# Optimization experiments

Measured on AMD Instinct MI355X. Metric: run time of the kernel, lower is better.

## Reference

```python
import jax, jax.numpy as jnp
import numpy as np

N_USERS = 60000
N_ITEMS = 30000
N_NODES = N_USERS + N_ITEMS
D = 64
L = 2


def _norm_adj(edge_index):
    # symmetrize: A_idx = [e, e.flip(0)]
    src = jnp.concatenate([edge_index[0], edge_index[1]])
    dst = jnp.concatenate([edge_index[1], edge_index[0]])
    ones = jnp.ones_like(src, dtype=jnp.float32)
    deg = jax.ops.segment_sum(ones, src, num_segments=N_NODES)
    deg = jnp.clip(deg, 1.0, None)
    val = jax.lax.rsqrt(deg[src]) * jax.lax.rsqrt(deg[dst])
    return src, dst, val


def _spmm(src, dst, val, x):
    # out[i] = sum_{(i,j) in E} val_ij * x[j]
    return jax.ops.segment_sum(val[:, None] * x[dst], src, num_segments=N_NODES)


def setup_inputs() -> dict:
    key = jax.random.key(0)
    ks = jax.random.split(key, 20)
    s = 0.02
    inp = {
        'x_txt': jax.random.normal(ks[0], (N_ITEMS, 768), jnp.float32),
        'x_img': jax.random.normal(ks[1], (N_ITEMS, 512), jnp.float32),
        'x_struct': jax.random.normal(ks[2], (N_ITEMS, 128), jnp.float32),
        'user_emb': jax.random.normal(ks[3], (3, N_USERS, D), jnp.float32) * s,
        'W_txt': jax.random.normal(ks[4], (3, 768, D), jnp.float32) * s,
        'b_txt': jax.random.normal(ks[5], (3, D), jnp.float32) * s,
        'W_img': jax.random.normal(ks[6], (3, 512, D), jnp.float32) * s,
        'b_img': jax.random.normal(ks[7], (3, D), jnp.float32) * s,
        'W_st': jax.random.normal(ks[8], (3, 128, D), jnp.float32) * s,
        'b_st': jax.random.normal(ks[9], (3, D), jnp.float32) * s,
        'Wu1': jax.random.normal(ks[10], (3 * D, 128), jnp.float32) * s,
        'bu1': jax.random.normal(ks[11], (128,), jnp.float32) * s,
        'Wu2': jax.random.normal(ks[12], (128, 3), jnp.float32) * s,
        'bu2': jax.random.normal(ks[13], (3,), jnp.float32) * s,
        'Wi1': jax.random.normal(ks[14], (3 * D, 128), jnp.float32) * s,
        'bi1': jax.random.normal(ks[15], (128,), jnp.float32) * s,
        'Wi2': jax.random.normal(ks[16], (128, 3), jnp.float32) * s,
        'bi2': jax.random.normal(ks[17], (3,), jnp.float32) * s,
        'edge_index': jax.random.randint(ks[18], (2, 500000), 0, N_NODES, jnp.int64),
    }
    return inp


def reference(x_txt, x_img, x_struct, user_emb, W_txt, b_txt, W_img, b_img,
              W_st, b_st, Wu1, bu1, Wu2, bu2, Wi1, bi1, Wi2, bi2, edge_index):
    src, dst, val = _norm_adj(edge_index)

    # item embeddings for all 3 branches at once: [n_items, 3, d]
    i0 = (jnp.einsum('nt,btd->nbd', x_txt, W_txt) + b_txt
          + jnp.einsum('nt,btd->nbd', x_img, W_img) + b_img
          + jnp.einsum('nt,btd->nbd', x_struct, W_st) + b_st)
    u0 = jnp.transpose(user_emb, (1, 0, 2))  # [n_users, 3, d]
    x = jnp.concatenate([u0, i0], axis=0).reshape(N_NODES, 3 * D)

    out = x
    for _ in range(L):
        x = _spmm(src, dst, val, x)
        out = out + x
    out = out / (L + 1)

    stack = out.reshape(N_NODES, 3, D)
    U_stack, I_stack = stack[:N_USERS], stack[N_USERS:]
    U_cat = U_stack.reshape(N_USERS, 3 * D)
    I_cat = I_stack.reshape(N_ITEMS, 3 * D)

    a_u = jax.nn.softmax(jax.nn.relu(U_cat @ Wu1 + bu1) @ Wu2 + bu2, axis=-1)
    a_i = jax.nn.softmax(jax.nn.relu(I_cat @ Wi1 + bi1) @ Wi2 + bi2, axis=-1)

    U = jnp.einsum('nb,nbd->nd', a_u, U_stack)
    I = jnp.einsum('nb,nbd->nd', a_i, I_stack)
    return jnp.concatenate([U, I], axis=0)  # [N_NODES, d]
```

## Files before the change

### kernel.cpp

```cpp
#include <hip/hip_runtime.h>
#include <math.h>

#define N_USERS 60000
#define N_ITEMS 30000
#define N_NODES 90000
#define DD 64
#define FF 192
#define FH 96
#define KK_TOT 1408
#define E_UND 500000
#define E_DIR 1000000
#define SCAN_NBLK 88

typedef __attribute__((ext_vector_type(8))) __bf16 bf16x8;
typedef __attribute__((ext_vector_type(8))) unsigned short u16x8;
typedef __attribute__((ext_vector_type(4))) float f32x4;

__device__ __forceinline__ unsigned short f2bf(float f) {
    unsigned int u = __float_as_uint(f);
    unsigned int r = (u + 0x7FFFu + ((u >> 16) & 1u)) >> 16;
    return (unsigned short)r;
}
__device__ __forceinline__ float bf_lo(unsigned int x) { return __uint_as_float(x << 16); }
__device__ __forceinline__ float bf_hi(unsigned int x) { return __uint_as_float(x & 0xFFFF0000u); }
__device__ __forceinline__ float bf2f(unsigned short x) {
    return __uint_as_float((unsigned int)x << 16);
}
__device__ __forceinline__ unsigned int pack2(float a, float b) {
    return ((unsigned int)f2bf(b) << 16) | (unsigned int)f2bf(a);
}

__global__ void k_mode(const int* __restrict__ ei, int* __restrict__ mode) {
    __shared__ int any;
    if (threadIdx.x == 0) any = 0;
    __syncthreads();
    if (ei[2 * threadIdx.x + 1] != 0) atomicOr(&any, 1);
    __syncthreads();
    if (threadIdx.x == 0) mode[0] = (any == 0) ? 1 : 0;
}

__device__ __forceinline__ void load_pair(const int* __restrict__ ei, int md, int u,
                                          int& a, int& b) {
    if (md) { a = ei[2 * u]; b = ei[2 * (E_UND + u)]; }
    else    { a = ei[u];     b = ei[E_UND + u]; }
}

__global__ void k_deg(const int* __restrict__ ei, const int* __restrict__ mode,
                      int* __restrict__ deg) {
    int i = blockIdx.x * 256 + threadIdx.x;
    if (i >= E_UND) return;
    int md = mode[0];
    int a, b;
    load_pair(ei, md, i, a, b);
    atomicAdd(&deg[a], 1);
    atomicAdd(&deg[b], 1);
}

__global__ __launch_bounds__(1024) void k_scan1(const int* __restrict__ deg,
                                                int* __restrict__ offs,
                                                int* __restrict__ bsum) {
    __shared__ int tmp[1024];
    int b = blockIdx.x, t = threadIdx.x;
    int i = b * 1024 + t;
    int v = (i < N_NODES) ? deg[i] : 0;
    tmp[t] = v;
    __syncthreads();
    for (int off = 1; off < 1024; off <<= 1) {
        int add = (t >= off) ? tmp[t - off] : 0;
        __syncthreads();
        tmp[t] += add;
        __syncthreads();
    }
    offs[i] = tmp[t] - v;
    if (t == 1023) bsum[b] = tmp[t];
}

__global__ void k_scan2(const int* __restrict__ bsum, int* __restrict__ bscan) {
    if (threadIdx.x == 0) {
        int run = 0;
        for (int b = 0; b < SCAN_NBLK; b++) { bscan[b] = run; run += bsum[b]; }
    }
}

__global__ void k_scan3(const int* __restrict__ deg, int* __restrict__ offs,
                        const int* __restrict__ bscan, int* __restrict__ cursor,
                        float* __restrict__ rsq) {
    int i = blockIdx.x * 256 + threadIdx.x;
    if (i >= N_NODES) return;
    int o = offs[i] + bscan[i >> 10];
    offs[i] = o;
    cursor[i] = o;
    int dg = deg[i];
    if (dg < 1) dg = 1;
    rsq[i] = rsqrtf((float)dg);
}

__global__ void k_fill(const int* __restrict__ ei, const int* __restrict__ mode,
                       int* __restrict__ cursor, const float* __restrict__ rsq,
                       int* __restrict__ edst, float* __restrict__ eval) {
    int i = blockIdx.x * 256 + threadIdx.x;
    if (i >= E_DIR) return;
    int md = mode[0];
    int u = (i < E_UND) ? i : i - E_UND;
    int a, b;
    load_pair(ei, md, u, a, b);
    int s, d;
    if (i < E_UND) { s = a; d = b; } else { s = b; d = a; }
    int slot = atomicAdd(&cursor[s], 1);
    edst[slot] = d;
    eval[slot] = rsq[s] * rsq[d];
}

__global__ void k_users(const float* __restrict__ ue, float* __restrict__ S) {
    int idx = blockIdx.x * 256 + threadIdx.x;
    if (idx >= N_USERS * FF) return;
    int n = idx / FF;
    int r = idx - n * FF;
    int b = r >> 6, d = r & 63;
    S[idx] = ue[((size_t)b * N_USERS + n) * DD + d];
}

__global__ void k_cvt_w(const float* __restrict__ Wt, const float* __restrict__ Wi,
                        const float* __restrict__ Wst, unsigned short* __restrict__ Wtb) {
    int idx = blockIdx.x * 256 + threadIdx.x;
    if (idx >= FF * KK_TOT) return;
    int n = idx / KK_TOT;
    int k = idx - n * KK_TOT;
    int b = n >> 6, d = n & 63;
    float v;
    if (k < 768)       v = Wt [((size_t)b * 768 + k) * 64 + d];
    else if (k < 1280) v = Wi [((size_t)b * 512 + (k - 768)) * 64 + d];
    else               v = Wst[((size_t)b * 128 + (k - 1280)) * 64 + d];
    Wtb[idx] = f2bf(v);
}

__global__ void k_cvt_w1(const float* __restrict__ Wu1, const float* __restrict__ Wi1,
                         unsigned short* __restrict__ W1Tu,
                         unsigned short* __restrict__ W1Ti) {
    int idx = blockIdx.x * 256 + threadIdx.x;
    if (idx >= 128 * FF) return;
    int n = idx / FF;
    int k = idx - n * FF;
    W1Tu[idx] = f2bf(Wu1[(size_t)k * 128 + n]);
    W1Ti[idx] = f2bf(Wi1[(size_t)k * 128 + n]);
}

#define BM 128
#define BN 64
#define BK 64
#define LDK 72

__global__ __launch_bounds__(256) void k_item_gemm_mfma(
    const float* __restrict__ xt, const float* __restrict__ xi, const float* __restrict__ xs,
    const unsigned short* __restrict__ Wtb,
    const float* __restrict__ bt, const float* __restrict__ bi, const float* __restrict__ bst,
    float* __restrict__ S) {
    __shared__ unsigned short Ash[BM * LDK];
    __shared__ unsigned short Bsh[BN * LDK];
    const int tid  = threadIdx.x;
    const int wave = tid >> 6;
    const int lane = tid & 63;
    const int row0 = blockIdx.x * BM;
    const int n0   = blockIdx.y * BN;

    f32x4 acc[2][4];
#pragma unroll
    for (int tm = 0; tm < 2; tm++)
#pragma unroll
        for (int tn = 0; tn < 4; tn++) acc[tm][tn] = (f32x4){0.f, 0.f, 0.f, 0.f};

    for (int k0 = 0; k0 < KK_TOT; k0 += BK) {
#pragma unroll
        for (int i = 0; i < 4; i++) {
            int id = tid + i * 256;
            int r = id >> 3;
            int c = (id & 7) << 3;
            int gr = row0 + r;
            int gk = k0 + c;
            float4 v0 = make_float4(0.f, 0.f, 0.f, 0.f);
            float4 v1 = v0;
            if (gr < N_ITEMS) {
                const float* src;
                int kl;
                if (gk < 768)       { src = xt + (size_t)gr * 768; kl = gk; }
                else if (gk < 1280) { src = xi + (size_t)gr * 512; kl = gk - 768; }
                else                { src = xs + (size_t)gr * 128; kl = gk - 1280; }
                v0 = *(const float4*)(src + kl);
                v1 = *(const float4*)(src + kl + 4);
            }
            u16x8 pk;
            pk[0] = f2bf(v0.x); pk[1] = f2bf(v0.y); pk[2] = f2bf(v0.z); pk[3] = f2bf(v0.w);
            pk[4] = f2bf(v1.x); pk[5] = f2bf(v1.y); pk[6] = f2bf(v1.z); pk[7] = f2bf(v1.w);
            *(u16x8*)(&Ash[r * LDK + c]) = pk;
        }
#pragma unroll
        for (int i = 0; i < 2; i++) {
            int id = tid + i * 256;
            int r = id >> 3;
            int c = (id & 7) << 3;
            *(u16x8*)(&Bsh[r * LDK + c]) =
                *(const u16x8*)(&Wtb[(size_t)(n0 + r) * KK_TOT + k0 + c]);
        }
        __syncthreads();
#pragma unroll
        for (int kk = 0; kk < BK; kk += 32) {
            bf16x8 af[2], bfr[4];
#pragma unroll
            for (int tm = 0; tm < 2; tm++)
                af[tm] = *(const bf16x8*)(&Ash[(wave * 32 + tm * 16 + (lane & 15)) * LDK +
                                               kk + (lane >> 4) * 8]);
#pragma unroll
            for (int tn = 0; tn < 4; tn++)
                bfr[tn] = *(const bf16x8*)(&Bsh[(tn * 16 + (lane & 15)) * LDK +
                                                kk + (lane >> 4) * 8]);
#pragma unroll
            for (int tm = 0; tm < 2; tm++)
#pragma unroll
                for (int tn = 0; tn < 4; tn++)
                    acc[tm][tn] = __builtin_amdgcn_mfma_f32_16x16x32_bf16(
                        af[tm], bfr[tn], acc[tm][tn], 0, 0, 0);
        }
        __syncthreads();
    }

    const int col16 = lane & 15;
    const int quad  = lane >> 4;
    const int b = blockIdx.y;
#pragma unroll
    for (int tn = 0; tn < 4; tn++) {
        int d = tn * 16 + col16;
        int n = n0 + d;
        float bias = bt[b * 64 + d] + bi[b * 64 + d] + bst[b * 64 + d];
#pragma unroll
        for (int tm = 0; tm < 2; tm++) {
#pragma unroll
            for (int r = 0; r < 4; r++) {
                int row = row0 + wave * 32 + tm * 16 + quad * 4 + r;
                if (row < N_ITEMS) {
                    S[(size_t)(N_USERS + row) * FF + n] = acc[tm][tn][r] + bias;
                }
            }
        }
    }
}

__global__ void k_pack(const float* __restrict__ S, unsigned int* __restrict__ Xb) {
    int i = blockIdx.x * 256 + threadIdx.x;
    if (i >= N_NODES * FH) return;
    float2 v = *(const float2*)(S + (size_t)i * 2);
    Xb[i] = pack2(v.x, v.y);
}

__global__ __launch_bounds__(192) void k_spmm_bf(const unsigned int* __restrict__ Xb,
                                                 unsigned int* __restrict__ Yb,
                                                 float* __restrict__ S,
                                                 const int* __restrict__ offs,
                                                 const int* __restrict__ deg,
                                                 const int* __restrict__ edst,
                                                 const float* __restrict__ eval) {
    int t = threadIdx.x;
    int half = (t >= FH) ? 1 : 0;
    int c = t - half * FH;
    int n = blockIdx.x * 2 + half;
    int start = offs[n];
    int dg = deg[n];
    const int* ed = edst + start;
    const float* ev = eval + start;
    float a0 = 0.f, a1 = 0.f;
    for (int j = 0; j < dg; j += 4) {
        int last = dg - 1;
        int j1 = (j + 1 < dg) ? j + 1 : last;
        int j2 = (j + 2 < dg) ? j + 2 : last;
        int j3 = (j + 3 < dg) ? j + 3 : last;
        int d0 = ed[j], d1 = ed[j1], d2 = ed[j2], d3 = ed[j3];
        float v0 = ev[j];
        float v1 = (j + 1 < dg) ? ev[j1] : 0.f;
        float v2 = (j + 2 < dg) ? ev[j2] : 0.f;
        float v3 = (j + 3 < dg) ? ev[j3] : 0.f;
        unsigned int x0 = Xb[(size_t)d0 * FH + c];
        unsigned int x1 = Xb[(size_t)d1 * FH + c];
        unsigned int x2 = Xb[(size_t)d2 * FH + c];
        unsigned int x3 = Xb[(size_t)d3 * FH + c];
        a0 = fmaf(v0, bf_lo(x0), a0); a1 = fmaf(v0, bf_hi(x0), a1);
        a0 = fmaf(v1, bf_lo(x1), a0); a1 = fmaf(v1, bf_hi(x1), a1);
        a0 = fmaf(v2, bf_lo(x2), a0); a1 = fmaf(v2, bf_hi(x2), a1);
        a0 = fmaf(v3, bf_lo(x3), a0); a1 = fmaf(v3, bf_hi(x3), a1);
    }
    size_t o = (size_t)n * FH + c;
    Yb[o] = pack2(a0, a1);
    float2* Sp = (float2*)(S + (size_t)n * FF);
    float2 s = Sp[c];
    s.x += a0; s.y += a1;
    Sp[c] = s;
}

#define LDA 200

__global__ __launch_bounds__(256) void k_attn_mfma(
    const float* __restrict__ S,
    const unsigned short* __restrict__ W1T,
    const float* __restrict__ B1,
    const float* __restrict__ W2,
    const float* __restrict__ B2,
    float* __restrict__ out,
    int node_base, int n_rows) {
    __shared__ unsigned short Atile[64 * LDA];
    __shared__ float aws[64][4];
    const int tid  = threadIdx.x;
    const int wave = tid >> 6;
    const int lane = tid & 63;
    const int row0 = blockIdx.x * 64;
    const float inv3 = 1.f / 3.f;

#pragma unroll
    for (int i = 0; i < 6; i++) {
        int id = tid + i * 256;
        int r = id / 24;
        int c = (id - r * 24) * 8;
        u16x8 pk;
        if (row0 + r < n_rows) {
            const float* src = S + (size_t)(node_base + row0 + r) * FF + c;
            float4 v0 = *(const float4*)(src);
            float4 v1 = *(const float4*)(src + 4);
            pk[0] = f2bf(v0.x * inv3); pk[1] = f2bf(v0.y * inv3);
            pk[2] = f2bf(v0.z * inv3); pk[3] = f2bf(v0.w * inv3);
            pk[4] = f2bf(v1.x * inv3); pk[5] = f2bf(v1.y * inv3);
            pk[6] = f2bf(v1.z * inv3); pk[7] = f2bf(v1.w * inv3);
        } else {
            pk = (u16x8){0, 0, 0, 0, 0, 0, 0, 0};
        }
        *(u16x8*)(&Atile[r * LDA + c]) = pk;
    }
    __syncthreads();

    f32x4 acc[8];
#pragma unroll
    for (int tn = 0; tn < 8; tn++) acc[tn] = (f32x4){0.f, 0.f, 0.f, 0.f};
    const int l16 = lane & 15;
    const int quad = lane >> 4;
#pragma unroll
    for (int kk = 0; kk < FF; kk += 32) {
        bf16x8 af = *(const bf16x8*)(&Atile[(wave * 16 + l16) * LDA + kk + quad * 8]);
#pragma unroll
        for (int tn = 0; tn < 8; tn++) {
            bf16x8 bf = *(const bf16x8*)(&W1T[(size_t)(tn * 16 + l16) * FF + kk + quad * 8]);
            acc[tn] = __builtin_amdgcn_mfma_f32_16x16x32_bf16(af, bf, acc[tn], 0, 0, 0);
        }
    }

    float pl[4][3];
#pragma unroll
    for (int r = 0; r < 4; r++) { pl[r][0] = 0.f; pl[r][1] = 0.f; pl[r][2] = 0.f; }
#pragma unroll
    for (int tn = 0; tn < 8; tn++) {
        int col = tn * 16 + l16;
        float b1v = B1[col];
        float w0 = W2[col * 3 + 0], w1 = W2[col * 3 + 1], w2v = W2[col * 3 + 2];
#pragma unroll
        for (int r = 0; r < 4; r++) {
            float h = fmaxf(acc[tn][r] + b1v, 0.f);
            pl[r][0] = fmaf(h, w0, pl[r][0]);
            pl[r][1] = fmaf(h, w1, pl[r][1]);
            pl[r][2] = fmaf(h, w2v, pl[r][2]);
        }
    }
#pragma unroll
    for (int m = 1; m <= 8; m <<= 1) {
#pragma unroll
        for (int r = 0; r < 4; r++) {
            pl[r][0] += __shfl_xor(pl[r][0], m, 64);
            pl[r][1] += __shfl_xor(pl[r][1], m, 64);
            pl[r][2] += __shfl_xor(pl[r][2], m, 64);
        }
    }
    float b20 = B2[0], b21 = B2[1], b22 = B2[2];
    if (l16 == 0) {
#pragma unroll
        for (int r = 0; r < 4; r++) {
            float l0 = pl[r][0] + b20, l1 = pl[r][1] + b21, l2 = pl[r][2] + b22;
            float mx = fmaxf(l0, fmaxf(l1, l2));
            float e0 = __expf(l0 - mx), e1 = __expf(l1 - mx), e2 = __expf(l2 - mx);
            float inv = 1.f / (e0 + e1 + e2);
            int rr = wave * 16 + quad * 4 + r;
            aws[rr][0] = e0 * inv; aws[rr][1] = e1 * inv; aws[rr][2] = e2 * inv;
        }
    }
    __syncthreads();

#pragma unroll
    for (int i = 0; i < 16; i++) {
        int flat = tid + i * 256;
        int r = flat >> 6, d = flat & 63;
        if (row0 + r < n_rows) {
            float a0 = aws[r][0], a1 = aws[r][1], a2 = aws[r][2];
            const unsigned short* Ar = &Atile[r * LDA];
            float v = a0 * bf2f(Ar[d]) + a1 * bf2f(Ar[64 + d]) + a2 * bf2f(Ar[128 + d]);
            out[(size_t)(node_base + row0 + r) * DD + d] = v;
        }
    }
}

extern "C" void kernel_launch(void* const* d_in, const int* in_sizes, int n_in,
                              void* d_out, int out_size, void* d_ws, size_t ws_size,
                              hipStream_t stream) {
    (void)in_sizes; (void)n_in; (void)out_size; (void)ws_size;
    const float* x_txt    = (const float*)d_in[0];
    const float* x_img    = (const float*)d_in[1];
    const float* x_struct = (const float*)d_in[2];
    const float* user_emb = (const float*)d_in[3];
    const float* W_txt    = (const float*)d_in[4];
    const float* b_txt    = (const float*)d_in[5];
    const float* W_img    = (const float*)d_in[6];
    const float* b_img    = (const float*)d_in[7];
    const float* W_st     = (const float*)d_in[8];
    const float* b_st     = (const float*)d_in[9];
    const float* Wu1      = (const float*)d_in[10];
    const float* bu1      = (const float*)d_in[11];
    const float* Wu2      = (const float*)d_in[12];
    const float* bu2      = (const float*)d_in[13];
    const float* Wi1      = (const float*)d_in[14];
    const float* bi1      = (const float*)d_in[15];
    const float* Wi2      = (const float*)d_in[16];
    const float* bi2      = (const float*)d_in[17];
    const int*   ei       = (const int*)d_in[18];
    float* out = (float*)d_out;

    char* base = (char*)d_ws;
    size_t off = 0;
    auto take = [&](size_t bytes) -> void* {
        void* p = base + off;
        off += (bytes + 255) & ~(size_t)255;
        return p;
    };
    float* S           = (float*)take((size_t)N_NODES * FF * 4);
    unsigned int* Xb0  = (unsigned int*)take((size_t)N_NODES * FH * 4);
    unsigned int* Yb   = (unsigned int*)take((size_t)N_NODES * FH * 4);
    int* deg    = (int*)take((size_t)N_NODES * 4);
    int* offs   = (int*)take((size_t)SCAN_NBLK * 1024 * 4);
    int* cursor = (int*)take((size_t)N_NODES * 4);
    int* bsum   = (int*)take((size_t)SCAN_NBLK * 4);
    int* bscan  = (int*)take((size_t)SCAN_NBLK * 4);
    float* rsq  = (float*)take((size_t)N_NODES * 4);
    int* edst   = (int*)take((size_t)E_DIR * 4);
    float* eval = (float*)take((size_t)E_DIR * 4);
    int* mode   = (int*)take(256);
    unsigned short* Wtb  = (unsigned short*)take((size_t)FF * KK_TOT * 2);
    unsigned short* W1Tu = (unsigned short*)take((size_t)128 * FF * 2);
    unsigned short* W1Ti = (unsigned short*)take((size_t)128 * FF * 2);

    hipMemsetAsync(deg, 0, (size_t)N_NODES * 4, stream);

    k_mode<<<1, 256, 0, stream>>>(ei, mode);
    k_deg<<<(E_UND + 255) / 256, 256, 0, stream>>>(ei, mode, deg);
    k_scan1<<<SCAN_NBLK, 1024, 0, stream>>>(deg, offs, bsum);
    k_scan2<<<1, 64, 0, stream>>>(bsum, bscan);
    k_scan3<<<(N_NODES + 255) / 256, 256, 0, stream>>>(deg, offs, bscan, cursor, rsq);
    k_fill<<<(E_DIR + 255) / 256, 256, 0, stream>>>(ei, mode, cursor, rsq, edst, eval);

    k_users<<<(N_USERS * FF + 255) / 256, 256, 0, stream>>>(user_emb, S);
    k_cvt_w<<<(FF * KK_TOT + 255) / 256, 256, 0, stream>>>(W_txt, W_img, W_st, Wtb);
    k_cvt_w1<<<(128 * FF + 255) / 256, 256, 0, stream>>>(Wu1, Wi1, W1Tu, W1Ti);
    k_item_gemm_mfma<<<dim3((N_ITEMS + BM - 1) / BM, 3), 256, 0, stream>>>(
        x_txt, x_img, x_struct, Wtb, b_txt, b_img, b_st, S);

    k_pack<<<(N_NODES * FH + 255) / 256, 256, 0, stream>>>(S, Xb0);
    k_spmm_bf<<<N_NODES / 2, 192, 0, stream>>>(Xb0, Yb, S, offs, deg, edst, eval);
    k_spmm_bf<<<N_NODES / 2, 192, 0, stream>>>(Yb, Xb0, S, offs, deg, edst, eval);

    k_attn_mfma<<<(N_USERS + 63) / 64, 256, 0, stream>>>(
        S, W1Tu, bu1, Wu2, bu2, out, 0, N_USERS);
    k_attn_mfma<<<(N_ITEMS + 63) / 64, 256, 0, stream>>>(
        S, W1Ti, bi1, Wi2, bi2, out, N_USERS, N_ITEMS);
}
```

Measured before the change: 684.5 us.

## Compute all three branches per item GEMM block and fuse bf16 packing into producers

The item GEMM now covers all 192 output columns in one block instead of launching three column blocks. Each fp32 input tile of text, image and structure features is therefore loaded and converted to bf16 once rather than three times. The user copy kernel and the GEMM epilogue also write the bf16 copy directly, which removes the separate pack kernel and its re-read of S. The cost is a much larger accumulator (24 MFMA tiles per wave), which raises register pressure and lowers occupancy, and the grid shrinks to about 235 blocks.

```diff
diff --git a/kernel.cpp b/kernel.cpp
--- a/kernel.cpp
+++ b/kernel.cpp
@@ -111,13 +111,16 @@
     eval[slot] = rsq[s] * rsq[d];
 }
 
-__global__ void k_users(const float* __restrict__ ue, float* __restrict__ S) {
+__global__ void k_users(const float* __restrict__ ue, float* __restrict__ S,
+                        unsigned short* __restrict__ Xbs) {
     int idx = blockIdx.x * 256 + threadIdx.x;
     if (idx >= N_USERS * FF) return;
     int n = idx / FF;
     int r = idx - n * FF;
     int b = r >> 6, d = r & 63;
-    S[idx] = ue[((size_t)b * N_USERS + n) * DD + d];
+    float v = ue[((size_t)b * N_USERS + n) * DD + d];
+    S[idx] = v;
+    Xbs[idx] = f2bf(v);
 }
 
 __global__ void k_cvt_w(const float* __restrict__ Wt, const float* __restrict__ Wi,
@@ -146,28 +149,26 @@
 }
 
 #define BM 128
-#define BN 64
 #define BK 64
 #define LDK 72
 
-__global__ __launch_bounds__(256) void k_item_gemm_mfma(
+__global__ __launch_bounds__(256) void k_item_gemm_mfma3(
     const float* __restrict__ xt, const float* __restrict__ xi, const float* __restrict__ xs,
     const unsigned short* __restrict__ Wtb,
     const float* __restrict__ bt, const float* __restrict__ bi, const float* __restrict__ bst,
-    float* __restrict__ S) {
+    float* __restrict__ S, unsigned short* __restrict__ Xbs) {
     __shared__ unsigned short Ash[BM * LDK];
-    __shared__ unsigned short Bsh[BN * LDK];
+    __shared__ unsigned short Bsh[FF * LDK];
     const int tid  = threadIdx.x;
     const int wave = tid >> 6;
     const int lane = tid & 63;
     const int row0 = blockIdx.x * BM;
-    const int n0   = blockIdx.y * BN;
-
-    f32x4 acc[2][4];
+
+    f32x4 acc[2][12];
 #pragma unroll
     for (int tm = 0; tm < 2; tm++)
 #pragma unroll
-        for (int tn = 0; tn < 4; tn++) acc[tm][tn] = (f32x4){0.f, 0.f, 0.f, 0.f};
+        for (int tn = 0; tn < 12; tn++) acc[tm][tn] = (f32x4){0.f, 0.f, 0.f, 0.f};
 
     for (int k0 = 0; k0 < KK_TOT; k0 += BK) {
 #pragma unroll
@@ -194,42 +195,40 @@
             *(u16x8*)(&Ash[r * LDK + c]) = pk;
         }
 #pragma unroll
-        for (int i = 0; i < 2; i++) {
+        for (int i = 0; i < 6; i++) {
             int id = tid + i * 256;
             int r = id >> 3;
             int c = (id & 7) << 3;
             *(u16x8*)(&Bsh[r * LDK + c]) =
-                *(const u16x8*)(&Wtb[(size_t)(n0 + r) * KK_TOT + k0 + c]);
+                *(const u16x8*)(&Wtb[(size_t)r * KK_TOT + k0 + c]);
         }
         __syncthreads();
 #pragma unroll
         for (int kk = 0; kk < BK; kk += 32) {
-            bf16x8 af[2], bfr[4];
+            bf16x8 af[2];
 #pragma unroll
             for (int tm = 0; tm < 2; tm++)
                 af[tm] = *(const bf16x8*)(&Ash[(wave * 32 + tm * 16 + (lane & 15)) * LDK +
                                                kk + (lane >> 4) * 8]);
 #pragma unroll
-            for (int tn = 0; tn < 4; tn++)
-                bfr[tn] = *(const bf16x8*)(&Bsh[(tn * 16 + (lane & 15)) * LDK +
-                                                kk + (lane >> 4) * 8]);
-#pragma unroll
-            for (int tm = 0; tm < 2; tm++)
-#pragma unroll
-                for (int tn = 0; tn < 4; tn++)
+            for (int tn = 0; tn < 12; tn++) {
+                bf16x8 bfr = *(const bf16x8*)(&Bsh[(tn * 16 + (lane & 15)) * LDK +
+                                                   kk + (lane >> 4) * 8]);
+#pragma unroll
+                for (int tm = 0; tm < 2; tm++)
                     acc[tm][tn] = __builtin_amdgcn_mfma_f32_16x16x32_bf16(
-                        af[tm], bfr[tn], acc[tm][tn], 0, 0, 0);
+                        af[tm], bfr, acc[tm][tn], 0, 0, 0);
+            }
         }
         __syncthreads();
     }
 
     const int col16 = lane & 15;
     const int quad  = lane >> 4;
-    const int b = blockIdx.y;
-#pragma unroll
-    for (int tn = 0; tn < 4; tn++) {
-        int d = tn * 16 + col16;
-        int n = n0 + d;
+#pragma unroll
+    for (int tn = 0; tn < 12; tn++) {
+        int n = tn * 16 + col16;
+        int b = n >> 6, d = n & 63;
         float bias = bt[b * 64 + d] + bi[b * 64 + d] + bst[b * 64 + d];
 #pragma unroll
         for (int tm = 0; tm < 2; tm++) {
@@ -237,18 +236,14 @@
             for (int r = 0; r < 4; r++) {
                 int row = row0 + wave * 32 + tm * 16 + quad * 4 + r;
                 if (row < N_ITEMS) {
-                    S[(size_t)(N_USERS + row) * FF + n] = acc[tm][tn][r] + bias;
+                    size_t o = (size_t)(N_USERS + row) * FF + n;
+                    float v = acc[tm][tn][r] + bias;
+                    S[o] = v;
+                    Xbs[o] = f2bf(v);
                 }
             }
         }
     }
-}
-
-__global__ void k_pack(const float* __restrict__ S, unsigned int* __restrict__ Xb) {
-    int i = blockIdx.x * 256 + threadIdx.x;
-    if (i >= N_NODES * FH) return;
-    float2 v = *(const float2*)(S + (size_t)i * 2);
-    Xb[i] = pack2(v.x, v.y);
 }
 
 __global__ __launch_bounds__(192) void k_spmm_bf(const unsigned int* __restrict__ Xb,
@@ -457,13 +452,13 @@
     k_scan3<<<(N_NODES + 255) / 256, 256, 0, stream>>>(deg, offs, bscan, cursor, rsq);
     k_fill<<<(E_DIR + 255) / 256, 256, 0, stream>>>(ei, mode, cursor, rsq, edst, eval);
 
-    k_users<<<(N_USERS * FF + 255) / 256, 256, 0, stream>>>(user_emb, S);
+    k_users<<<(N_USERS * FF + 255) / 256, 256, 0, stream>>>(user_emb, S,
+                                                            (unsigned short*)Xb0);
     k_cvt_w<<<(FF * KK_TOT + 255) / 256, 256, 0, stream>>>(W_txt, W_img, W_st, Wtb);
     k_cvt_w1<<<(128 * FF + 255) / 256, 256, 0, stream>>>(Wu1, Wi1, W1Tu, W1Ti);
-    k_item_gemm_mfma<<<dim3((N_ITEMS + BM - 1) / BM, 3), 256, 0, stream>>>(
-        x_txt, x_img, x_struct, Wtb, b_txt, b_img, b_st, S);
-
-    k_pack<<<(N_NODES * FH + 255) / 256, 256, 0, stream>>>(S, Xb0);
+    k_item_gemm_mfma3<<<(N_ITEMS + BM - 1) / BM, 256, 0, stream>>>(
+        x_txt, x_img, x_struct, Wtb, b_txt, b_img, b_st, S, (unsigned short*)Xb0);
+
     k_spmm_bf<<<N_NODES / 2, 192, 0, stream>>>(Xb0, Yb, S, offs, deg, edst, eval);
     k_spmm_bf<<<N_NODES / 2, 192, 0, stream>>>(Yb, Xb0, S, offs, deg, edst, eval);
 
```

Result: no change. 697.2 us (+1.9%).
